# Performance work log

Measured on AMD Instinct MI355X. Metric: run time of the kernel, lower is better.

## Reference

```python
import jax, jax.numpy as jnp
import numpy as np
from functools import partial

MAX_DEPTH = 100.0
MIN_DEPTH = 0.1
KS = 5  # custom_kernel_size


def _dilate(x, k):
    # max_pool2d(x, k, stride=1, padding=k//2); torch pads with -inf for max pool
    p = k // 2
    return jax.lax.reduce_window(x, -jnp.inf, jax.lax.max,
                                 (1, 1, k, k), (1, 1, 1, 1),
                                 [(0, 0), (0, 0), (p, p), (p, p)])


def _erode(x, k):
    return -_dilate(-x, k)


def _median_blur(x, k):
    # torch impl: conv2d with identity kernels (zero padding) then median over window dim
    p = k // 2
    b, c, h, w = x.shape
    xp = jnp.pad(x, ((0, 0), (0, 0), (p, p), (p, p)))  # zeros, matching conv2d padding
    wins = jnp.stack([xp[:, :, i:i + h, j:j + w]
                      for i in range(k) for j in range(k)], axis=2)  # [b,c,k*k,h,w]
    return jnp.median(wins, axis=2)


def _gaussian_blur5(x):
    # torchvision gaussian_blur(kernel_size=5, sigma=None):
    # sigma = 0.3*((5-1)*0.5 - 1) + 0.8 = 1.1, reflect padding
    sigma = 1.1
    r = jnp.arange(5, dtype=x.dtype) - 2.0
    g1 = jnp.exp(-(r ** 2) / (2.0 * sigma ** 2))
    g1 = g1 / jnp.sum(g1)
    g2 = jnp.outer(g1, g1)  # [5,5]
    xp = jnp.pad(x, ((0, 0), (0, 0), (2, 2), (2, 2)), mode='reflect')
    kern = g2[None, None]  # [O=1, I=1, 5, 5]
    return jax.lax.conv_general_dilated(xp, kern, (1, 1), 'VALID',
                                        dimension_numbers=('NCHW', 'OIHW', 'NCHW'))


def setup_inputs() -> dict:
    key = jax.random.key(0)
    k1, k2 = jax.random.split(key)
    depth = jax.random.uniform(k1, (16, 1, 352, 1216), dtype=jnp.float32) * MAX_DEPTH
    mask = jax.random.uniform(k2, (16, 1, 352, 1216)) < 0.3
    in_depth = jnp.where(mask, depth, 0.0).astype(jnp.float32)
    return {"in_depth": in_depth}


def reference(in_depth):
    # invert
    dm = jnp.where(in_depth > MIN_DEPTH, MAX_DEPTH - in_depth, in_depth)
    # dilation with custom kernel
    dm = _dilate(dm, KS)
    # closing(5) = erode(dilate)
    dm = _erode(_dilate(dm, 5), 5)
    # fill empty pixels with 7x7 dilation
    empty = dm < MIN_DEPTH
    dm = jnp.where(empty, _dilate(dm, 7), dm)
    # median blur 5
    dm = _median_blur(dm, 5)
    # gaussian blur 5 on valid pixels
    blurred = _gaussian_blur5(dm)
    dm = jnp.where(dm > MIN_DEPTH, blurred, dm)
    # invert back
    dm = jnp.where(dm > MIN_DEPTH, MAX_DEPTH - dm, dm)
    return dm
```

## Files before the change

### kernel.cpp

```cpp
#include <hip/hip_runtime.h>
#include <float.h>
#include <math.h>

#define IW 1216
#define IH 352
#define W4 304
#define MIND 0.1f
#define MAXD 100.0f
#define RB 50

__device__ __forceinline__ float4 vmax4(float4 a, float4 b) {
    return make_float4(fmaxf(a.x,b.x), fmaxf(a.y,b.y), fmaxf(a.z,b.z), fmaxf(a.w,b.w));
}
__device__ __forceinline__ float4 vmin4(float4 a, float4 b) {
    return make_float4(fminf(a.x,b.x), fminf(a.y,b.y), fminf(a.z,b.z), fminf(a.w,b.w));
}

#define CE(a,b) { float _l = fminf(a,b), _h = fmaxf(a,b); a = _l; b = _h; }
#define SORT5(a,b,c,d,e) { CE(a,b) CE(d,e) CE(c,e) CE(c,d) CE(a,d) CE(a,c) CE(b,e) CE(b,d) CE(b,c) }
#define MM8(s0,s1,s2,s3,s4,s5,s6,s7) { CE(s0,s1) CE(s2,s3) CE(s4,s5) CE(s6,s7) \
    CE(s0,s2) CE(s0,s4) CE(s0,s6) CE(s1,s7) CE(s3,s7) CE(s5,s7) }
#define MM7(s0,s1,s2,s3,s4,s5,s6) { CE(s0,s1) CE(s2,s3) CE(s4,s5) \
    CE(s0,s2) CE(s0,s4) CE(s0,s6) CE(s1,s6) CE(s3,s6) CE(s5,s6) }

__global__ __launch_bounds__(256, 2) void mega_k(const float4* __restrict__ in,
                                                 float4* __restrict__ out,
                                                 float w0, float w1, float w2) {
    __shared__ float4 A_[RB][40];
    __shared__ float4 B_[RB][38];
    int b  = blockIdx.x;
    int sw = (b & 7) * 300 + (b >> 3);
    int tx = sw % 10; int t2 = sw / 10;
    int ty = t2 % 15; int n  = t2 / 15;
    int x0 = tx * 128, y0 = ty * 24;
    int tid = threadIdx.x;
    const long ib = (long)n * (IH * W4);
    const int xb4 = x0 >> 2;

    for (int i = tid; i < 50 * 40; i += 256) {
        int ra = i / 40, ca = i % 40;
        int gy = y0 + ra - 13, gx4 = xb4 + ca - 4;
        float4 v;
        if ((unsigned)gy < IH && (unsigned)gx4 < W4) {
            v = in[ib + gy * W4 + gx4];
            v.x = v.x > MIND ? MAXD - v.x : v.x;
            v.y = v.y > MIND ? MAXD - v.y : v.y;
            v.z = v.z > MIND ? MAXD - v.z : v.z;
            v.w = v.w > MIND ? MAXD - v.w : v.w;
        } else { v.x = v.y = v.z = v.w = -FLT_MAX; }
        A_[ra][ca] = v;
    }
    __syncthreads();

    for (int i = tid; i < 50 * 38; i += 256) {
        int ra = i / 38, cb = i % 38;
        float t[12];
        *(float4*)&t[0] = A_[ra][cb];
        *(float4*)&t[4] = A_[ra][cb + 1];
        *(float4*)&t[8] = A_[ra][cb + 2];
        float core = fmaxf(fmaxf(fmaxf(t[3],t[4]), fmaxf(t[5],t[6])), fmaxf(t[7],t[8]));
        float a12 = fmaxf(t[1], t[2]), a910 = fmaxf(t[9], t[10]);
        float4 o;
        o.x = fmaxf(fmaxf(core, a12), t[0]);
        o.y = fmaxf(fmaxf(core, a12), t[9]);
        o.z = fmaxf(fmaxf(core, t[2]), a910);
        o.w = fmaxf(fmaxf(core, a910), t[11]);
        B_[ra][cb] = o;
    }
    __syncthreads();

    {
        int c = tid % 38, k = tid / 38;
        if (k < 6) {
            int ra0 = 4 + 7 * k;
            float4 w[9];
            #pragma unroll
            for (int j = 0; j < 8; ++j) w[j] = B_[ra0 - 4 + j][c];
            #pragma unroll
            for (int s = 0; s < 7; ++s) {
                w[8] = B_[ra0 + 4 + s][c];
                float4 m = w[0];
                #pragma unroll
                for (int j = 1; j < 9; ++j) m = vmax4(m, w[j]);
                A_[ra0 + s][c + 1] = m;
                #pragma unroll
                for (int j = 0; j < 8; ++j) w[j] = w[j + 1];
            }
        }
    }
    __syncthreads();

    for (int i = tid; i < 42 * 36; i += 256) {
        int ra = i / 36 + 4, cb = i % 36;
        float t[12];
        *(float4*)&t[0] = A_[ra][cb + 1];
        *(float4*)&t[4] = A_[ra][cb + 2];
        *(float4*)&t[8] = A_[ra][cb + 3];
        bool rOK = (unsigned)(y0 + ra - 13) < IH;
        #pragma unroll
        for (int kk = 2; kk <= 9; ++kk) {
            int gx = x0 + 4 * cb - 12 + kk;
            t[kk] = (rOK && (unsigned)gx < IW) ? t[kk] : FLT_MAX;
        }
        float m34 = fminf(t[3], t[4]), m56 = fminf(t[5], t[6]), m78 = fminf(t[7], t[8]);
        float4 o;
        o.x = fminf(fminf(t[2], m34), m56);
        o.y = fminf(fminf(m34, m56), t[7]);
        o.z = fminf(fminf(t[4], m56), m78);
        o.w = fminf(fminf(m56, m78), t[9]);
        B_[ra][cb + 1] = o;
    }
    __syncthreads();

    {
        int c = tid % 36, k = tid / 36;
        if (k < 7) {
            int ra0 = 6 + 6 * k;
            int rlen = min(6, 44 - ra0);
            float4 w[5];
            #pragma unroll
            for (int j = 0; j < 4; ++j) w[j] = B_[ra0 - 2 + j][c + 1];
            #pragma unroll
            for (int s = 0; s < 6; ++s) {
                if (s < rlen) {
                    w[4] = B_[ra0 + 2 + s][c + 1];
                    float4 m = w[0];
                    #pragma unroll
                    for (int j = 1; j < 5; ++j) m = vmin4(m, w[j]);
                    A_[ra0 + s][c + 2] = m;
                    #pragma unroll
                    for (int j = 0; j < 4; ++j) w[j] = w[j + 1];
                }
            }
        }
    }
    __syncthreads();

    for (int i = tid; i < 38 * 34; i += 256) {
        int ra = i / 34 + 6, cb2 = i % 34;
        float t[12];
        *(float4*)&t[0] = A_[ra][cb2 + 2];
        *(float4*)&t[4] = A_[ra][cb2 + 3];
        *(float4*)&t[8] = A_[ra][cb2 + 4];
        bool rOK = (unsigned)(y0 + ra - 13) < IH;
        #pragma unroll
        for (int kk = 1; kk <= 10; ++kk) {
            int gx = x0 + 4 * cb2 - 8 + kk;
            t[kk] = (rOK && (unsigned)gx < IW) ? t[kk] : -FLT_MAX;
        }
        float core = fmaxf(fmaxf(t[4], t[5]), fmaxf(t[6], t[7]));
        float a23 = fmaxf(t[2], t[3]), a89 = fmaxf(t[8], t[9]);
        float4 o;
        o.x = fmaxf(fmaxf(core, a23), t[1]);
        o.y = fmaxf(fmaxf(core, a23), t[8]);
        o.z = fmaxf(fmaxf(core, t[3]), a89);
        o.w = fmaxf(fmaxf(core, a89), t[10]);
        B_[ra][cb2 + 2] = o;
    }
    __syncthreads();

    {
        int c = tid % 34, k = tid / 34;
        if (k < 7) {
            int ra0 = 9 + 5 * k;
            int rlen = min(5, 41 - ra0);
            float4 w[7];
            #pragma unroll
            for (int j = 0; j < 6; ++j) w[j] = B_[ra0 - 3 + j][c + 2];
            #pragma unroll
            for (int s = 0; s < 5; ++s) {
                if (s < rlen) {
                    w[6] = B_[ra0 + 3 + s][c + 2];
                    float4 m = w[0];
                    #pragma unroll
                    for (int j = 1; j < 7; ++j) m = vmax4(m, w[j]);
                    float4 cl = A_[ra0 + s][c + 3];
                    float4 o;
                    o.x = cl.x < MIND ? m.x : cl.x;
                    o.y = cl.y < MIND ? m.y : cl.y;
                    o.z = cl.z < MIND ? m.z : cl.z;
                    o.w = cl.w < MIND ? m.w : cl.w;
                    A_[ra0 + s][c + 3] = o;
                    #pragma unroll
                    for (int j = 0; j < 6; ++j) w[j] = w[j + 1];
                }
            }
        }
    }
    __syncthreads();

    {
        int c = tid % 34, k = tid / 34;
        if (k < 7) {
            int ra0 = 11 + 4 * k;
            float rows_[5][8];
            auto loadrow = [&](float* rw, int rr) {
                float4 q0 = A_[rr][c + 2], q1 = A_[rr][c + 3], q2 = A_[rr][c + 4];
                float tmp[8] = {q0.z, q0.w, q1.x, q1.y, q1.z, q1.w, q2.x, q2.y};
                bool rOK = (unsigned)(y0 + rr - 13) < IH;
                #pragma unroll
                for (int j = 0; j < 8; ++j) {
                    int gx = x0 + 4 * c - 6 + j;
                    rw[j] = (rOK && (unsigned)gx < IW) ? tmp[j] : 0.0f;
                }
            };
            #pragma unroll
            for (int j = 0; j < 4; ++j) loadrow(rows_[j], ra0 - 2 + j);
            #pragma unroll
            for (int st = 0; st < 4; ++st) {
                loadrow(rows_[4], ra0 + 2 + st);
                float cs[8][5];
                #pragma unroll
                for (int j = 0; j < 8; ++j) {
                    float a0 = rows_[0][j], a1 = rows_[1][j], a2 = rows_[2][j],
                          a3 = rows_[3][j], a4 = rows_[4][j];
                    SORT5(a0, a1, a2, a3, a4)
                    cs[j][0] = a0; cs[j][1] = a1; cs[j][2] = a2; cs[j][3] = a3; cs[j][4] = a4;
                }
                float rr4[4];
                #pragma unroll
                for (int p = 0; p < 4; ++p) {
                    float m[5][5];
                    #pragma unroll
                    for (int i2 = 0; i2 < 5; ++i2) {
                        m[i2][0] = cs[p][i2];     m[i2][1] = cs[p + 1][i2];
                        m[i2][2] = cs[p + 2][i2]; m[i2][3] = cs[p + 3][i2];
                        m[i2][4] = cs[p + 4][i2];
                        SORT5(m[i2][0], m[i2][1], m[i2][2], m[i2][3], m[i2][4])
                    }
                    float s0 = m[0][3], s1 = m[0][4], s2 = m[1][2], s3 = m[1][3];
                    float s4 = m[1][4], s5 = m[2][1], s6 = m[2][2], s7 = m[2][3];
                    MM8(s0, s1, s2, s3, s4, s5, s6, s7)
                    s0 = m[3][0]; s7 = m[3][1];
                    MM8(s0, s1, s2, s3, s4, s5, s6, s7)
                    s0 = m[3][2]; s7 = m[4][0];
                    MM8(s0, s1, s2, s3, s4, s5, s6, s7)
                    s0 = m[4][1];
                    MM7(s0, s1, s2, s3, s4, s5, s6)
                    CE(s1, s2) CE(s3, s4) CE(s1, s3) CE(s2, s4)
                    float mn = fminf(s2, s3), mx = fmaxf(s2, s3);
                    rr4[p] = fmaxf(mn, fminf(mx, s5));
                }
                B_[ra0 + st][c + 2] = make_float4(rr4[0], rr4[1], rr4[2], rr4[3]);
                #pragma unroll
                for (int j = 0; j < 4; ++j) {
                    #pragma unroll
                    for (int q = 0; q < 8; ++q) rows_[j][q] = rows_[j + 1][q];
                }
            }
        }
    }
    __syncthreads();

    for (int i = tid; i < 28 * 32; i += 256) {
        int ra = i / 32 + 11, cb3 = i % 32;
        float t[12];
        *(float4*)&t[0] = B_[ra][cb3 + 2];
        *(float4*)&t[4] = B_[ra][cb3 + 3];
        *(float4*)&t[8] = B_[ra][cb3 + 4];
        if (x0 == 0 && cb3 == 0)      { t[2] = t[6]; t[3] = t[5]; }
        if (x0 == 1152 && cb3 == 15)  { t[8] = t[6]; t[9] = t[5]; }
        float4 o;
        o.x = w2 * (t[2] + t[6]) + w1 * (t[3] + t[5]) + w0 * t[4];
        o.y = w2 * (t[3] + t[7]) + w1 * (t[4] + t[6]) + w0 * t[5];
        o.z = w2 * (t[4] + t[8]) + w1 * (t[5] + t[7]) + w0 * t[6];
        o.w = w2 * (t[5] + t[9]) + w1 * (t[6] + t[8]) + w0 * t[7];
        A_[ra][cb3 + 4] = o;
    }
    __syncthreads();

    {
        int c = tid % 32, k = tid / 32;
        int ra0 = 13 + 3 * k;
        #pragma unroll
        for (int s = 0; s < 3; ++s) {
            int ra = ra0 + s;
            int gy = y0 + ra - 13;
            float4 acc = make_float4(0.f, 0.f, 0.f, 0.f);
            #pragma unroll
            for (int d = -2; d <= 2; ++d) {
                int gy2 = gy + d;
                gy2 = gy2 < 0 ? -gy2 : gy2;
                gy2 = gy2 >= IH ? 2 * IH - 2 - gy2 : gy2;
                int ra2 = gy2 - y0 + 13;
                float4 hv = A_[ra2][c + 4];
                float wd = (d == 0) ? w0 : ((d == 1 || d == -1) ? w1 : w2);
                acc.x = fmaf(wd, hv.x, acc.x); acc.y = fmaf(wd, hv.y, acc.y);
                acc.z = fmaf(wd, hv.z, acc.z); acc.w = fmaf(wd, hv.w, acc.w);
            }
            float4 dm = B_[ra][c + 3];
            float4 o;
            { float sv = dm.x > MIND ? acc.x : dm.x; o.x = sv > MIND ? MAXD - sv : sv; }
            { float sv = dm.y > MIND ? acc.y : dm.y; o.y = sv > MIND ? MAXD - sv : sv; }
            { float sv = dm.z > MIND ? acc.z : dm.z; o.z = sv > MIND ? MAXD - sv : sv; }
            { float sv = dm.w > MIND ? acc.w : dm.w; o.w = sv > MIND ? MAXD - sv : sv; }
            int gx4 = xb4 + c;
            if (gy < IH && gx4 < W4) out[ib + (long)gy * W4 + gx4] = o;
        }
    }
}

extern "C" void kernel_launch(void* const* d_in, const int* in_sizes, int n_in,
                              void* d_out, int out_size, void* d_ws, size_t ws_size,
                              hipStream_t stream) {
    const float4* in = (const float4*)d_in[0];
    float4* O = (float4*)d_out;

    float c2 = 2.42f;
    float e1 = expf(-1.0f / c2);
    float e4 = expf(-4.0f / c2);
    float s  = 1.0f + 2.0f * e1 + 2.0f * e4;
    float w0 = 1.0f / s, w1 = e1 / s, w2 = e4 / s;

    mega_k<<<dim3(2400), dim3(256), 0, stream>>>(in, O, w0, w1, w2);
}
```

Before: 182.3 us.

## Shrink tile height to 16 rows, raise occupancy, add interior fast path

The output tile height drops from 24 to 16 rows, which shrinks the shared-memory footprint and lets the launch bound ask for 3 blocks per CU instead of 2. Every stage's row partition is retuned to match, and the grid grows from 2400 to 3520 blocks. Interior tiles now skip the per-element boundary masking in the load, erode, dilate and median stages. In exchange, the 13-row halo is a larger share of each tile, so more redundant halo loads and recomputation happen per output pixel.

```diff
diff --git a/kernel.cpp b/kernel.cpp
--- a/kernel.cpp
+++ b/kernel.cpp
@@ -7,7 +7,7 @@
 #define W4 304
 #define MIND 0.1f
 #define MAXD 100.0f
-#define RB 50
+#define RB 42
 
 __device__ __forceinline__ float4 vmax4(float4 a, float4 b) {
     return make_float4(fmaxf(a.x,b.x), fmaxf(a.y,b.y), fmaxf(a.z,b.z), fmaxf(a.w,b.w));
@@ -23,36 +23,50 @@
 #define MM7(s0,s1,s2,s3,s4,s5,s6) { CE(s0,s1) CE(s2,s3) CE(s4,s5) \
     CE(s0,s2) CE(s0,s4) CE(s0,s6) CE(s1,s6) CE(s3,s6) CE(s5,s6) }
 
-__global__ __launch_bounds__(256, 2) void mega_k(const float4* __restrict__ in,
+__global__ __launch_bounds__(256, 3) void mega_k(const float4* __restrict__ in,
                                                  float4* __restrict__ out,
                                                  float w0, float w1, float w2) {
-    __shared__ float4 A_[RB][40];
-    __shared__ float4 B_[RB][38];
+    __shared__ float4 A_[RB][41];
+    __shared__ float4 B_[RB][39];
     int b  = blockIdx.x;
-    int sw = (b & 7) * 300 + (b >> 3);
+    int sw = (b & 7) * 440 + (b >> 3);
     int tx = sw % 10; int t2 = sw / 10;
-    int ty = t2 % 15; int n  = t2 / 15;
-    int x0 = tx * 128, y0 = ty * 24;
+    int ty = t2 % 22; int n  = t2 / 22;
+    int x0 = tx * 128, y0 = ty * 16;
     int tid = threadIdx.x;
     const long ib = (long)n * (IH * W4);
     const int xb4 = x0 >> 2;
-
-    for (int i = tid; i < 50 * 40; i += 256) {
-        int ra = i / 40, ca = i % 40;
-        int gy = y0 + ra - 13, gx4 = xb4 + ca - 4;
-        float4 v;
-        if ((unsigned)gy < IH && (unsigned)gx4 < W4) {
-            v = in[ib + gy * W4 + gx4];
+    const bool interior = (tx >= 1) && (tx <= 8) && (ty >= 1) && (ty <= 20);
+
+    if (interior) {
+        for (int i = tid; i < RB * 40; i += 256) {
+            int ra = i / 40, ca = i % 40;
+            int gy = y0 + ra - 13, gx4 = xb4 + ca - 4;
+            float4 v = in[ib + gy * W4 + gx4];
             v.x = v.x > MIND ? MAXD - v.x : v.x;
             v.y = v.y > MIND ? MAXD - v.y : v.y;
             v.z = v.z > MIND ? MAXD - v.z : v.z;
             v.w = v.w > MIND ? MAXD - v.w : v.w;
-        } else { v.x = v.y = v.z = v.w = -FLT_MAX; }
-        A_[ra][ca] = v;
-    }
-    __syncthreads();
-
-    for (int i = tid; i < 50 * 38; i += 256) {
+            A_[ra][ca] = v;
+        }
+    } else {
+        for (int i = tid; i < RB * 40; i += 256) {
+            int ra = i / 40, ca = i % 40;
+            int gy = y0 + ra - 13, gx4 = xb4 + ca - 4;
+            float4 v;
+            if ((unsigned)gy < IH && (unsigned)gx4 < W4) {
+                v = in[ib + gy * W4 + gx4];
+                v.x = v.x > MIND ? MAXD - v.x : v.x;
+                v.y = v.y > MIND ? MAXD - v.y : v.y;
+                v.z = v.z > MIND ? MAXD - v.z : v.z;
+                v.w = v.w > MIND ? MAXD - v.w : v.w;
+            } else { v.x = v.y = v.z = v.w = -FLT_MAX; }
+            A_[ra][ca] = v;
+        }
+    }
+    __syncthreads();
+
+    for (int i = tid; i < RB * 38; i += 256) {
         int ra = i / 38, cb = i % 38;
         float t[12];
         *(float4*)&t[0] = A_[ra][cb];
@@ -72,35 +86,39 @@
     {
         int c = tid % 38, k = tid / 38;
         if (k < 6) {
-            int ra0 = 4 + 7 * k;
+            int ra0 = 4 + 6 * k;
             float4 w[9];
             #pragma unroll
             for (int j = 0; j < 8; ++j) w[j] = B_[ra0 - 4 + j][c];
             #pragma unroll
-            for (int s = 0; s < 7; ++s) {
-                w[8] = B_[ra0 + 4 + s][c];
-                float4 m = w[0];
-                #pragma unroll
-                for (int j = 1; j < 9; ++j) m = vmax4(m, w[j]);
-                A_[ra0 + s][c + 1] = m;
-                #pragma unroll
-                for (int j = 0; j < 8; ++j) w[j] = w[j + 1];
-            }
-        }
-    }
-    __syncthreads();
-
-    for (int i = tid; i < 42 * 36; i += 256) {
+            for (int s = 0; s < 6; ++s) {
+                if (ra0 + s <= 37) {
+                    w[8] = B_[ra0 + 4 + s][c];
+                    float4 m = w[0];
+                    #pragma unroll
+                    for (int j = 1; j < 9; ++j) m = vmax4(m, w[j]);
+                    A_[ra0 + s][c + 1] = m;
+                    #pragma unroll
+                    for (int j = 0; j < 8; ++j) w[j] = w[j + 1];
+                }
+            }
+        }
+    }
+    __syncthreads();
+
+    for (int i = tid; i < 34 * 36; i += 256) {
         int ra = i / 36 + 4, cb = i % 36;
         float t[12];
         *(float4*)&t[0] = A_[ra][cb + 1];
         *(float4*)&t[4] = A_[ra][cb + 2];
         *(float4*)&t[8] = A_[ra][cb + 3];
-        bool rOK = (unsigned)(y0 + ra - 13) < IH;
-        #pragma unroll
-        for (int kk = 2; kk <= 9; ++kk) {
-            int gx = x0 + 4 * cb - 12 + kk;
-            t[kk] = (rOK && (unsigned)gx < IW) ? t[kk] : FLT_MAX;
+        if (!interior) {
+            bool rOK = (unsigned)(y0 + ra - 13) < IH;
+            #pragma unroll
+            for (int kk = 2; kk <= 9; ++kk) {
+                int gx = x0 + 4 * cb - 12 + kk;
+                t[kk] = (rOK && (unsigned)gx < IW) ? t[kk] : FLT_MAX;
+            }
         }
         float m34 = fminf(t[3], t[4]), m56 = fminf(t[5], t[6]), m78 = fminf(t[7], t[8]);
         float4 o;
@@ -114,39 +132,38 @@
 
     {
         int c = tid % 36, k = tid / 36;
-        if (k < 7) {
-            int ra0 = 6 + 6 * k;
-            int rlen = min(6, 44 - ra0);
+        if (k < 6) {
+            int ra0 = 6 + 5 * k;
             float4 w[5];
             #pragma unroll
             for (int j = 0; j < 4; ++j) w[j] = B_[ra0 - 2 + j][c + 1];
             #pragma unroll
-            for (int s = 0; s < 6; ++s) {
-                if (s < rlen) {
-                    w[4] = B_[ra0 + 2 + s][c + 1];
-                    float4 m = w[0];
-                    #pragma unroll
-                    for (int j = 1; j < 5; ++j) m = vmin4(m, w[j]);
-                    A_[ra0 + s][c + 2] = m;
-                    #pragma unroll
-                    for (int j = 0; j < 4; ++j) w[j] = w[j + 1];
-                }
-            }
-        }
-    }
-    __syncthreads();
-
-    for (int i = tid; i < 38 * 34; i += 256) {
+            for (int s = 0; s < 5; ++s) {
+                w[4] = B_[ra0 + 2 + s][c + 1];
+                float4 m = w[0];
+                #pragma unroll
+                for (int j = 1; j < 5; ++j) m = vmin4(m, w[j]);
+                A_[ra0 + s][c + 2] = m;
+                #pragma unroll
+                for (int j = 0; j < 4; ++j) w[j] = w[j + 1];
+            }
+        }
+    }
+    __syncthreads();
+
+    for (int i = tid; i < 30 * 34; i += 256) {
         int ra = i / 34 + 6, cb2 = i % 34;
         float t[12];
         *(float4*)&t[0] = A_[ra][cb2 + 2];
         *(float4*)&t[4] = A_[ra][cb2 + 3];
         *(float4*)&t[8] = A_[ra][cb2 + 4];
-        bool rOK = (unsigned)(y0 + ra - 13) < IH;
-        #pragma unroll
-        for (int kk = 1; kk <= 10; ++kk) {
-            int gx = x0 + 4 * cb2 - 8 + kk;
-            t[kk] = (rOK && (unsigned)gx < IW) ? t[kk] : -FLT_MAX;
+        if (!interior) {
+            bool rOK = (unsigned)(y0 + ra - 13) < IH;
+            #pragma unroll
+            for (int kk = 1; kk <= 10; ++kk) {
+                int gx = x0 + 4 * cb2 - 8 + kk;
+                t[kk] = (rOK && (unsigned)gx < IW) ? t[kk] : -FLT_MAX;
+            }
         }
         float core = fmaxf(fmaxf(t[4], t[5]), fmaxf(t[6], t[7]));
         float a23 = fmaxf(t[2], t[3]), a89 = fmaxf(t[8], t[9]);
@@ -161,29 +178,26 @@
 
     {
         int c = tid % 34, k = tid / 34;
-        if (k < 7) {
-            int ra0 = 9 + 5 * k;
-            int rlen = min(5, 41 - ra0);
+        if (k < 6) {
+            int ra0 = 9 + 4 * k;
             float4 w[7];
             #pragma unroll
             for (int j = 0; j < 6; ++j) w[j] = B_[ra0 - 3 + j][c + 2];
             #pragma unroll
-            for (int s = 0; s < 5; ++s) {
-                if (s < rlen) {
-                    w[6] = B_[ra0 + 3 + s][c + 2];
-                    float4 m = w[0];
-                    #pragma unroll
-                    for (int j = 1; j < 7; ++j) m = vmax4(m, w[j]);
-                    float4 cl = A_[ra0 + s][c + 3];
-                    float4 o;
-                    o.x = cl.x < MIND ? m.x : cl.x;
-                    o.y = cl.y < MIND ? m.y : cl.y;
-                    o.z = cl.z < MIND ? m.z : cl.z;
-                    o.w = cl.w < MIND ? m.w : cl.w;
-                    A_[ra0 + s][c + 3] = o;
-                    #pragma unroll
-                    for (int j = 0; j < 6; ++j) w[j] = w[j + 1];
-                }
+            for (int s = 0; s < 4; ++s) {
+                w[6] = B_[ra0 + 3 + s][c + 2];
+                float4 m = w[0];
+                #pragma unroll
+                for (int j = 1; j < 7; ++j) m = vmax4(m, w[j]);
+                float4 cl = A_[ra0 + s][c + 3];
+                float4 o;
+                o.x = cl.x < MIND ? m.x : cl.x;
+                o.y = cl.y < MIND ? m.y : cl.y;
+                o.z = cl.z < MIND ? m.z : cl.z;
+                o.w = cl.w < MIND ? m.w : cl.w;
+                A_[ra0 + s][c + 3] = o;
+                #pragma unroll
+                for (int j = 0; j < 6; ++j) w[j] = w[j + 1];
             }
         }
     }
@@ -192,67 +206,75 @@
     {
         int c = tid % 34, k = tid / 34;
         if (k < 7) {
-            int ra0 = 11 + 4 * k;
+            int ra0 = 11 + 3 * k;
+            int rlen = min(3, 31 - ra0);
             float rows_[5][8];
             auto loadrow = [&](float* rw, int rr) {
                 float4 q0 = A_[rr][c + 2], q1 = A_[rr][c + 3], q2 = A_[rr][c + 4];
                 float tmp[8] = {q0.z, q0.w, q1.x, q1.y, q1.z, q1.w, q2.x, q2.y};
-                bool rOK = (unsigned)(y0 + rr - 13) < IH;
-                #pragma unroll
-                for (int j = 0; j < 8; ++j) {
-                    int gx = x0 + 4 * c - 6 + j;
-                    rw[j] = (rOK && (unsigned)gx < IW) ? tmp[j] : 0.0f;
+                if (interior) {
+                    #pragma unroll
+                    for (int j = 0; j < 8; ++j) rw[j] = tmp[j];
+                } else {
+                    bool rOK = (unsigned)(y0 + rr - 13) < IH;
+                    #pragma unroll
+                    for (int j = 0; j < 8; ++j) {
+                        int gx = x0 + 4 * c - 6 + j;
+                        rw[j] = (rOK && (unsigned)gx < IW) ? tmp[j] : 0.0f;
+                    }
                 }
             };
             #pragma unroll
             for (int j = 0; j < 4; ++j) loadrow(rows_[j], ra0 - 2 + j);
             #pragma unroll
-            for (int st = 0; st < 4; ++st) {
-                loadrow(rows_[4], ra0 + 2 + st);
-                float cs[8][5];
-                #pragma unroll
-                for (int j = 0; j < 8; ++j) {
-                    float a0 = rows_[0][j], a1 = rows_[1][j], a2 = rows_[2][j],
-                          a3 = rows_[3][j], a4 = rows_[4][j];
-                    SORT5(a0, a1, a2, a3, a4)
-                    cs[j][0] = a0; cs[j][1] = a1; cs[j][2] = a2; cs[j][3] = a3; cs[j][4] = a4;
+            for (int st = 0; st < 3; ++st) {
+                if (st < rlen) {
+                    loadrow(rows_[4], ra0 + 2 + st);
+                    float cs[8][5];
+                    #pragma unroll
+                    for (int j = 0; j < 8; ++j) {
+                        float a0 = rows_[0][j], a1 = rows_[1][j], a2 = rows_[2][j],
+                              a3 = rows_[3][j], a4 = rows_[4][j];
+                        SORT5(a0, a1, a2, a3, a4)
+                        cs[j][0] = a0; cs[j][1] = a1; cs[j][2] = a2; cs[j][3] = a3; cs[j][4] = a4;
+                    }
+                    float rr4[4];
+                    #pragma unroll
+                    for (int p = 0; p < 4; ++p) {
+                        float m[5][5];
+                        #pragma unroll
+                        for (int i2 = 0; i2 < 5; ++i2) {
+                            m[i2][0] = cs[p][i2];     m[i2][1] = cs[p + 1][i2];
+                            m[i2][2] = cs[p + 2][i2]; m[i2][3] = cs[p + 3][i2];
+                            m[i2][4] = cs[p + 4][i2];
+                            SORT5(m[i2][0], m[i2][1], m[i2][2], m[i2][3], m[i2][4])
+                        }
+                        float s0 = m[0][3], s1 = m[0][4], s2 = m[1][2], s3 = m[1][3];
+                        float s4 = m[1][4], s5 = m[2][1], s6 = m[2][2], s7 = m[2][3];
+                        MM8(s0, s1, s2, s3, s4, s5, s6, s7)
+                        s0 = m[3][0]; s7 = m[3][1];
+                        MM8(s0, s1, s2, s3, s4, s5, s6, s7)
+                        s0 = m[3][2]; s7 = m[4][0];
+                        MM8(s0, s1, s2, s3, s4, s5, s6, s7)
+                        s0 = m[4][1];
+                        MM7(s0, s1, s2, s3, s4, s5, s6)
+                        CE(s1, s2) CE(s3, s4) CE(s1, s3) CE(s2, s4)
+                        float mn = fminf(s2, s3), mx = fmaxf(s2, s3);
+                        rr4[p] = fmaxf(mn, fminf(mx, s5));
+                    }
+                    B_[ra0 + st][c + 2] = make_float4(rr4[0], rr4[1], rr4[2], rr4[3]);
+                    #pragma unroll
+                    for (int j = 0; j < 4; ++j) {
+                        #pragma unroll
+                        for (int q = 0; q < 8; ++q) rows_[j][q] = rows_[j + 1][q];
+                    }
                 }
-                float rr4[4];
-                #pragma unroll
-                for (int p = 0; p < 4; ++p) {
-                    float m[5][5];
-                    #pragma unroll
-                    for (int i2 = 0; i2 < 5; ++i2) {
-                        m[i2][0] = cs[p][i2];     m[i2][1] = cs[p + 1][i2];
-                        m[i2][2] = cs[p + 2][i2]; m[i2][3] = cs[p + 3][i2];
-                        m[i2][4] = cs[p + 4][i2];
-                        SORT5(m[i2][0], m[i2][1], m[i2][2], m[i2][3], m[i2][4])
-                    }
-                    float s0 = m[0][3], s1 = m[0][4], s2 = m[1][2], s3 = m[1][3];
-                    float s4 = m[1][4], s5 = m[2][1], s6 = m[2][2], s7 = m[2][3];
-                    MM8(s0, s1, s2, s3, s4, s5, s6, s7)
-                    s0 = m[3][0]; s7 = m[3][1];
-                    MM8(s0, s1, s2, s3, s4, s5, s6, s7)
-                    s0 = m[3][2]; s7 = m[4][0];
-                    MM8(s0, s1, s2, s3, s4, s5, s6, s7)
-                    s0 = m[4][1];
-                    MM7(s0, s1, s2, s3, s4, s5, s6)
-                    CE(s1, s2) CE(s3, s4) CE(s1, s3) CE(s2, s4)
-                    float mn = fminf(s2, s3), mx = fmaxf(s2, s3);
-                    rr4[p] = fmaxf(mn, fminf(mx, s5));
-                }
-                B_[ra0 + st][c + 2] = make_float4(rr4[0], rr4[1], rr4[2], rr4[3]);
-                #pragma unroll
-                for (int j = 0; j < 4; ++j) {
-                    #pragma unroll
-                    for (int q = 0; q < 8; ++q) rows_[j][q] = rows_[j + 1][q];
-                }
-            }
-        }
-    }
-    __syncthreads();
-
-    for (int i = tid; i < 28 * 32; i += 256) {
+            }
+        }
+    }
+    __syncthreads();
+
+    for (int i = tid; i < 20 * 32; i += 256) {
         int ra = i / 32 + 11, cb3 = i % 32;
         float t[12];
         *(float4*)&t[0] = B_[ra][cb3 + 2];
@@ -271,9 +293,9 @@
 
     {
         int c = tid % 32, k = tid / 32;
-        int ra0 = 13 + 3 * k;
+        int ra0 = 13 + 2 * k;
         #pragma unroll
-        for (int s = 0; s < 3; ++s) {
+        for (int s = 0; s < 2; ++s) {
             int ra = ra0 + s;
             int gy = y0 + ra - 13;
             float4 acc = make_float4(0.f, 0.f, 0.f, 0.f);
@@ -295,7 +317,7 @@
             { float sv = dm.z > MIND ? acc.z : dm.z; o.z = sv > MIND ? MAXD - sv : sv; }
             { float sv = dm.w > MIND ? acc.w : dm.w; o.w = sv > MIND ? MAXD - sv : sv; }
             int gx4 = xb4 + c;
-            if (gy < IH && gx4 < W4) out[ib + (long)gy * W4 + gx4] = o;
+            if (gx4 < W4) out[ib + (long)gy * W4 + gx4] = o;
         }
     }
 }
@@ -312,5 +334,5 @@
     float s  = 1.0f + 2.0f * e1 + 2.0f * e4;
     float w0 = 1.0f / s, w1 = e1 / s, w2 = e4 / s;
 
-    mega_k<<<dim3(2400), dim3(256), 0, stream>>>(in, O, w0, w1, w2);
+    mega_k<<<dim3(3520), dim3(256), 0, stream>>>(in, O, w0, w1, w2);
 }
```

New measurement: 176.8 us. -3.0%, faster.
